# Kernel optimization log

Hardware: AMD Instinct MI355X
Metric: run time of the kernel (lower is better)

The kernel has to match this reference:

```python
import jax, jax.numpy as jnp
import numpy as np

B, T, M, D, O = 32, 4096, 256, 257, 40


def _make_cum_matrix():
    # 0/1 indicator: phone m covers a contiguous run of frames (segment-sum operator)
    seg_ids = (np.arange(T) * M) // T            # (T,) frame -> phone id
    ind = (seg_ids[None, :] == np.arange(M)[:, None]).astype(np.float32)  # (M,T)
    return jnp.broadcast_to(jnp.asarray(ind), (B, M, T))


def setup_inputs() -> dict:
    key = jax.random.key(0)
    k1, k2, k3, k4 = jax.random.split(key, 4)
    x = jax.random.normal(k1, (B, T, D), dtype=jnp.float32)
    # 0/1 phone-activity mask per frame/phone-class (as used via abs() in torch code)
    batch_target_phones = (jax.random.uniform(k2, (B, T, O)) < 0.5).astype(jnp.float32)
    batch_cum_matrix = _make_cum_matrix()
    W = jax.random.normal(k3, (O, D), dtype=jnp.float32) * 0.05
    b = jax.random.normal(k4, (O,), dtype=jnp.float32) * 0.05
    return {"x": x, "batch_target_phones": batch_target_phones,
            "batch_cum_matrix": batch_cum_matrix, "W": W, "b": b}


def reference(x, batch_target_phones, batch_cum_matrix, W, b):
    # summarize='mean' (generic non-'min' branch), loss_per_phone=True, eval=False
    # n_frames per phone, scattered back to frames as an extra feature column
    n_frames_by_phone = jnp.sum(batch_cum_matrix, axis=2)                     # (B, M)
    n_frames_2frame = jnp.einsum('bmt,bm->bt', batch_cum_matrix,
                                 n_frames_by_phone)[..., None]                # (B, T, 1)
    feats = jnp.concatenate([x[:, :, 1:], n_frames_2frame], axis=-1)          # (B, T, 257)
    out = jnp.einsum('btd,od->bto', feats, W) + b                             # (B, T, 40)
    masked = out * jnp.abs(batch_target_phones)                               # (B, T, 40)
    summed = jnp.einsum('bmt,bto->bmo', batch_cum_matrix, masked)             # (B, M, 40)
    frame_counts = jnp.einsum('bmt,bto->bmo', batch_cum_matrix,
                              batch_target_phones)                            # (B, M, 40)
    frame_counts = jnp.where(frame_counts == 0, 1.0, frame_counts)
    return summed / frame_counts                                              # (B, M, 40)
```

## Files before the change

### kernel.cpp

```cpp
#include <hip/hip_runtime.h>


#define B_  32
#define T_  4096
#define M_  256
#define D_  257
#define O_  40

#define NT    256
#define FPB   64
#define NSLOT 24

typedef float f32x4 __attribute__((ext_vector_type(4)));
typedef f32x4 f32x4u __attribute__((aligned(4)));
typedef _Float16 f16x8 __attribute__((ext_vector_type(8)));

__global__ __launch_bounds__(NT, 4) void ftdnn_mfma3(
    const float* __restrict__ x,
    const float* __restrict__ tp,
    const float* __restrict__ W,
    const float* __restrict__ bias,
    float* __restrict__ out)
{
    __shared__ __align__(16) _Float16 ws[NSLOT * 64 * 8];

    const int tid  = threadIdx.x;
    const int b    = blockIdx.y;
    const int mg   = blockIdx.x;
    const int lane = tid & 63;
    const int wv   = tid >> 6;
    const int ra   = lane & 15;
    const int kg   = lane >> 4;
    const int seg  = mg * 4 + wv;

    const float* xp = x + ((size_t)b * T_ + (size_t)seg * 16 + ra) * D_ + 1 + kg * 8;
    f32x4 xv[16];
#pragma unroll
    for (int kk = 0; kk < 8; ++kk) {
        const f32x4u* pv = reinterpret_cast<const f32x4u*>(xp + kk * 32);
        xv[2 * kk]     = pv[0];
        xv[2 * kk + 1] = pv[1];
    }
    const float* tpb = tp + ((size_t)b * T_ + (size_t)seg * 16) * O_;
    float tpv[3][4];
#pragma unroll
    for (int n = 0; n < 3; ++n) {
        const int o = n * 16 + ra;
#pragma unroll
        for (int r = 0; r < 4; ++r) {
            const int tl = kg * 4 + r;
            tpv[n][r] = (o < O_) ? tpb[(size_t)tl * O_ + o] : 0.f;
        }
    }
    float wcv[3], bsv[3];
#pragma unroll
    for (int n = 0; n < 3; ++n) {
        const int o = n * 16 + ra;
        wcv[n] = (o < O_) ? W[(size_t)o * D_ + 256] : 0.f;
        bsv[n] = (o < O_) ? bias[o] : 0.f;
    }

    for (int fid = tid; fid < NSLOT * 64; fid += NT) {
        const int slot = fid >> 6;
        const int ln   = fid & 63;
        const int n    = slot >> 3;
        const int kk   = slot & 7;
        const int o    = n * 16 + (ln & 15);
        const int k0   = kk * 32 + (ln >> 4) * 8;
        f16x8 h;
        if (o < O_) {
            const f32x4u* p = reinterpret_cast<const f32x4u*>(W + (size_t)o * D_ + k0);
            f32x4 d0 = p[0], d1 = p[1];
#pragma unroll
            for (int q = 0; q < 4; ++q) {
                h[q]     = (_Float16)d0[q];
                h[4 + q] = (_Float16)d1[q];
            }
        } else {
#pragma unroll
            for (int q = 0; q < 8; ++q) h[q] = (_Float16)0.f;
        }
        *reinterpret_cast<f16x8*>(&ws[fid * 8]) = h;
    }
    __syncthreads();

    const f16x8* wfrag = reinterpret_cast<const f16x8*>(ws);

    f32x4 acc[3];
#pragma unroll
    for (int n = 0; n < 3; ++n)
#pragma unroll
        for (int r = 0; r < 4; ++r) acc[n][r] = 0.f;

#pragma unroll
    for (int kk = 0; kk < 8; ++kk) {
        f32x4 d0 = xv[2 * kk];
        f32x4 d1 = xv[2 * kk + 1];
        f16x8 ah, al;
#pragma unroll
        for (int q = 0; q < 4; ++q) {
            ah[q]     = (_Float16)d0[q];
            al[q]     = (_Float16)(d0[q] - (float)ah[q]);
            ah[4 + q] = (_Float16)d1[q];
            al[4 + q] = (_Float16)(d1[q] - (float)ah[4 + q]);
        }
#pragma unroll
        for (int n = 0; n < 3; ++n) {
            f16x8 bh = wfrag[(n * 8 + kk) * 64 + lane];
            acc[n] = __builtin_amdgcn_mfma_f32_16x16x32_f16(ah, bh, acc[n], 0, 0, 0);
            acc[n] = __builtin_amdgcn_mfma_f32_16x16x32_f16(al, bh, acc[n], 0, 0, 0);
        }
    }

#pragma unroll
    for (int n = 0; n < 3; ++n) {
        const int o = n * 16 + ra;
        float s = 0.f, cnt = 0.f;
#pragma unroll
        for (int r = 0; r < 4; ++r) {
            s = fmaf(tpv[n][r], acc[n][r], s);
            cnt += tpv[n][r];
        }
        s   += __shfl_xor(s, 16);
        s   += __shfl_xor(s, 32);
        cnt += __shfl_xor(cnt, 16);
        cnt += __shfl_xor(cnt, 32);
        if (lane < 16 && o < O_) {
            float c     = fmaf(16.f, wcv[n], bsv[n]);
            float denom = (cnt == 0.f) ? 1.f : cnt;
            out[((size_t)b * M_ + seg) * O_ + o] = fmaf(c, cnt, s) / denom;
        }
    }
}

extern "C" void kernel_launch(void* const* d_in, const int* in_sizes, int n_in,
                              void* d_out, int out_size, void* d_ws, size_t ws_size,
                              hipStream_t stream) {
    const float* x    = (const float*)d_in[0];
    const float* tp   = (const float*)d_in[1];
    const float* W    = (const float*)d_in[3];
    const float* bias = (const float*)d_in[4];
    float* out        = (float*)d_out;

    dim3 grid(T_ / FPB, B_);
    dim3 block(NT);
    ftdnn_mfma3<<<grid, block, 0, stream>>>(x, tp, W, bias, out);
}
```

Measured before the change: 36.59 us.

## Process two segments per wave with software-pipelined x loads

Each wave now handles two 16-frame segments instead of one, which halves the grid and spreads the per-block W conversion into LDS over twice as much work. The x loads for the second segment are issued in halves while the MFMAs for the first segment run, overlapping global memory latency with compute. The cost is fewer blocks (1024 vs 2048), which lowers parallelism and occupancy headroom, plus slightly higher register pressure.

```diff
diff --git a/kernel.cpp b/kernel.cpp
--- a/kernel.cpp
+++ b/kernel.cpp
@@ -8,14 +8,13 @@
 #define O_  40
 
 #define NT    256
-#define FPB   64
 #define NSLOT 24
 
 typedef float f32x4 __attribute__((ext_vector_type(4)));
 typedef f32x4 f32x4u __attribute__((aligned(4)));
 typedef _Float16 f16x8 __attribute__((ext_vector_type(8)));
 
-__global__ __launch_bounds__(NT, 4) void ftdnn_mfma3(
+__global__ __launch_bounds__(NT, 4) void ftdnn_mfma4(
     const float* __restrict__ x,
     const float* __restrict__ tp,
     const float* __restrict__ W,
@@ -31,26 +30,29 @@
     const int wv   = tid >> 6;
     const int ra   = lane & 15;
     const int kg   = lane >> 4;
-    const int seg  = mg * 4 + wv;
+    const int s0   = mg * 8 + wv * 2;
 
-    const float* xp = x + ((size_t)b * T_ + (size_t)seg * 16 + ra) * D_ + 1 + kg * 8;
-    f32x4 xv[16];
+    const float* xp  = x + ((size_t)b * T_ + (size_t)s0 * 16 + ra) * D_ + 1 + kg * 8;
+    const float* tpb = tp + ((size_t)b * T_ + (size_t)s0 * 16) * O_;
+
+    f32x4 a0[8], a1[8];
 #pragma unroll
-    for (int kk = 0; kk < 8; ++kk) {
-        const f32x4u* pv = reinterpret_cast<const f32x4u*>(xp + kk * 32);
-        xv[2 * kk]     = pv[0];
-        xv[2 * kk + 1] = pv[1];
+    for (int i = 0; i < 4; ++i) {
+        const f32x4u* pv = reinterpret_cast<const f32x4u*>(xp + i * 32);
+        a0[2 * i] = pv[0];  a0[2 * i + 1] = pv[1];
     }
-    const float* tpb = tp + ((size_t)b * T_ + (size_t)seg * 16) * O_;
+#pragma unroll
+    for (int i = 0; i < 4; ++i) {
+        const f32x4u* pv = reinterpret_cast<const f32x4u*>(xp + 128 + i * 32);
+        a1[2 * i] = pv[0];  a1[2 * i + 1] = pv[1];
+    }
     float tpv[3][4];
 #pragma unroll
     for (int n = 0; n < 3; ++n) {
         const int o = n * 16 + ra;
 #pragma unroll
-        for (int r = 0; r < 4; ++r) {
-            const int tl = kg * 4 + r;
-            tpv[n][r] = (o < O_) ? tpb[(size_t)tl * O_ + o] : 0.f;
-        }
+        for (int r = 0; r < 4; ++r)
+            tpv[n][r] = (o < O_) ? tpb[(size_t)(kg * 4 + r) * O_ + o] : 0.f;
     }
     float wcv[3], bsv[3];
 #pragma unroll
@@ -86,51 +88,90 @@
 
     const f16x8* wfrag = reinterpret_cast<const f16x8*>(ws);
 
+    auto do_half = [&](const f32x4* av, int kkb, f32x4 (&acc)[3]) {
+#pragma unroll
+        for (int j = 0; j < 4; ++j) {
+            const int kk = kkb + j;
+            f32x4 d0 = av[2 * j];
+            f32x4 d1 = av[2 * j + 1];
+            f16x8 ah, al;
+#pragma unroll
+            for (int q = 0; q < 4; ++q) {
+                ah[q]     = (_Float16)d0[q];
+                al[q]     = (_Float16)(d0[q] - (float)ah[q]);
+                ah[4 + q] = (_Float16)d1[q];
+                al[4 + q] = (_Float16)(d1[q] - (float)ah[4 + q]);
+            }
+#pragma unroll
+            for (int n = 0; n < 3; ++n) {
+                f16x8 bh = wfrag[(n * 8 + kk) * 64 + lane];
+                acc[n] = __builtin_amdgcn_mfma_f32_16x16x32_f16(ah, bh, acc[n], 0, 0, 0);
+                acc[n] = __builtin_amdgcn_mfma_f32_16x16x32_f16(al, bh, acc[n], 0, 0, 0);
+            }
+        }
+    };
+
+    auto epilogue = [&](int seg, const f32x4 (&acc)[3], const float (&tpm)[3][4]) {
+#pragma unroll
+        for (int n = 0; n < 3; ++n) {
+            const int o = n * 16 + ra;
+            float s = 0.f, cnt = 0.f;
+#pragma unroll
+            for (int r = 0; r < 4; ++r) {
+                s = fmaf(tpm[n][r], acc[n][r], s);
+                cnt += tpm[n][r];
+            }
+            s   += __shfl_xor(s, 16);
+            s   += __shfl_xor(s, 32);
+            cnt += __shfl_xor(cnt, 16);
+            cnt += __shfl_xor(cnt, 32);
+            if (lane < 16 && o < O_) {
+                float c     = fmaf(16.f, wcv[n], bsv[n]);
+                float denom = (cnt == 0.f) ? 1.f : cnt;
+                out[((size_t)b * M_ + seg) * O_ + o] = fmaf(c, cnt, s) / denom;
+            }
+        }
+    };
+
     f32x4 acc[3];
 #pragma unroll
     for (int n = 0; n < 3; ++n)
 #pragma unroll
         for (int r = 0; r < 4; ++r) acc[n][r] = 0.f;
 
+    const float* xq = xp + (size_t)16 * D_;
+
+    do_half(a0, 0, acc);
 #pragma unroll
-    for (int kk = 0; kk < 8; ++kk) {
-        f32x4 d0 = xv[2 * kk];
-        f32x4 d1 = xv[2 * kk + 1];
-        f16x8 ah, al;
+    for (int i = 0; i < 4; ++i) {
+        const f32x4u* pv = reinterpret_cast<const f32x4u*>(xq + i * 32);
+        a0[2 * i] = pv[0];  a0[2 * i + 1] = pv[1];
+    }
+    do_half(a1, 4, acc);
 #pragma unroll
-        for (int q = 0; q < 4; ++q) {
-            ah[q]     = (_Float16)d0[q];
-            al[q]     = (_Float16)(d0[q] - (float)ah[q]);
-            ah[4 + q] = (_Float16)d1[q];
-            al[4 + q] = (_Float16)(d1[q] - (float)ah[4 + q]);
-        }
+    for (int i = 0; i < 4; ++i) {
+        const f32x4u* pv = reinterpret_cast<const f32x4u*>(xq + 128 + i * 32);
+        a1[2 * i] = pv[0];  a1[2 * i + 1] = pv[1];
+    }
+    epilogue(s0, acc, tpv);
+
+    const float* tpb1 = tpb + (size_t)16 * O_;
 #pragma unroll
-        for (int n = 0; n < 3; ++n) {
-            f16x8 bh = wfrag[(n * 8 + kk) * 64 + lane];
-            acc[n] = __builtin_amdgcn_mfma_f32_16x16x32_f16(ah, bh, acc[n], 0, 0, 0);
-            acc[n] = __builtin_amdgcn_mfma_f32_16x16x32_f16(al, bh, acc[n], 0, 0, 0);
-        }
+    for (int n = 0; n < 3; ++n) {
+        const int o = n * 16 + ra;
+#pragma unroll
+        for (int r = 0; r < 4; ++r)
+            tpv[n][r] = (o < O_) ? tpb1[(size_t)(kg * 4 + r) * O_ + o] : 0.f;
     }
 
 #pragma unroll
-    for (int n = 0; n < 3; ++n) {
-        const int o = n * 16 + ra;
-        float s = 0.f, cnt = 0.f;
+    for (int n = 0; n < 3; ++n)
 #pragma unroll
-        for (int r = 0; r < 4; ++r) {
-            s = fmaf(tpv[n][r], acc[n][r], s);
-            cnt += tpv[n][r];
-        }
-        s   += __shfl_xor(s, 16);
-        s   += __shfl_xor(s, 32);
-        cnt += __shfl_xor(cnt, 16);
-        cnt += __shfl_xor(cnt, 32);
-        if (lane < 16 && o < O_) {
-            float c     = fmaf(16.f, wcv[n], bsv[n]);
-            float denom = (cnt == 0.f) ? 1.f : cnt;
-            out[((size_t)b * M_ + seg) * O_ + o] = fmaf(c, cnt, s) / denom;
-        }
-    }
+        for (int r = 0; r < 4; ++r) acc[n][r] = 0.f;
+
+    do_half(a0, 0, acc);
+    do_half(a1, 4, acc);
+    epilogue(s0 + 1, acc, tpv);
 }
 
 extern "C" void kernel_launch(void* const* d_in, const int* in_sizes, int n_in,
@@ -142,7 +183,7 @@
     const float* bias = (const float*)d_in[4];
     float* out        = (float*)d_out;
 
-    dim3 grid(T_ / FPB, B_);
+    dim3 grid(32, 32);
     dim3 block(NT);
-    ftdnn_mfma3<<<grid, block, 0, stream>>>(x, tp, W, bias, out);
+    ftdnn_mfma4<<<grid, block, 0, stream>>>(x, tp, W, bias, out);
 }
```

After: 32.58 us. -11.0%, faster.

## Process two segments per wave with coalesced x loads staged through LDS and prefetch

Applied to the files above, without the earlier changes.

Each wave now handles two 16-frame segments instead of one, which halves the grid and amortizes the per-block W-to-fp16 staging. Rows of x are loaded with a more coalesced pattern (8 lanes per row, 4 floats each), split into hi/lo fp16 and written to per-wave LDS tiles, then read back in MFMA fragment layout. The next segment's x is prefetched while the current MFMAs run, and tp loads are moved late in the loop. The cost is extra LDS traffic, the wave-local LDS write/read ordering it depends on, and fewer blocks available to hide latency.

```diff
diff --git a/kernel.cpp b/kernel.cpp
--- a/kernel.cpp
+++ b/kernel.cpp
@@ -8,14 +8,16 @@
 #define O_  40
 
 #define NT    256
-#define FPB   64
+#define SEGW  2
 #define NSLOT 24
+#define XROWP 40
 
 typedef float f32x4 __attribute__((ext_vector_type(4)));
 typedef f32x4 f32x4u __attribute__((aligned(4)));
 typedef _Float16 f16x8 __attribute__((ext_vector_type(8)));
+typedef _Float16 f16x4 __attribute__((ext_vector_type(4)));
 
-__global__ __launch_bounds__(NT, 4) void ftdnn_mfma3(
+__global__ __launch_bounds__(NT, 4) void ftdnn_mfma6(
     const float* __restrict__ x,
     const float* __restrict__ tp,
     const float* __restrict__ W,
@@ -23,6 +25,8 @@
     float* __restrict__ out)
 {
     __shared__ __align__(16) _Float16 ws[NSLOT * 64 * 8];
+    __shared__ __align__(16) _Float16 xhi[4][16 * XROWP];
+    __shared__ __align__(16) _Float16 xlo[4][16 * XROWP];
 
     const int tid  = threadIdx.x;
     const int b    = blockIdx.y;
@@ -31,36 +35,11 @@
     const int wv   = tid >> 6;
     const int ra   = lane & 15;
     const int kg   = lane >> 4;
-    const int seg  = mg * 4 + wv;
+    const int s0   = mg * 8 + wv * 2;
 
-    const float* xp = x + ((size_t)b * T_ + (size_t)seg * 16 + ra) * D_ + 1 + kg * 8;
-    f32x4 xv[16];
 #pragma unroll
-    for (int kk = 0; kk < 8; ++kk) {
-        const f32x4u* pv = reinterpret_cast<const f32x4u*>(xp + kk * 32);
-        xv[2 * kk]     = pv[0];
-        xv[2 * kk + 1] = pv[1];
-    }
-    const float* tpb = tp + ((size_t)b * T_ + (size_t)seg * 16) * O_;
-    float tpv[3][4];
-#pragma unroll
-    for (int n = 0; n < 3; ++n) {
-        const int o = n * 16 + ra;
-#pragma unroll
-        for (int r = 0; r < 4; ++r) {
-            const int tl = kg * 4 + r;
-            tpv[n][r] = (o < O_) ? tpb[(size_t)tl * O_ + o] : 0.f;
-        }
-    }
-    float wcv[3], bsv[3];
-#pragma unroll
-    for (int n = 0; n < 3; ++n) {
-        const int o = n * 16 + ra;
-        wcv[n] = (o < O_) ? W[(size_t)o * D_ + 256] : 0.f;
-        bsv[n] = (o < O_) ? bias[o] : 0.f;
-    }
-
-    for (int fid = tid; fid < NSLOT * 64; fid += NT) {
+    for (int it = 0; it < 6; ++it) {
+        const int fid  = tid + it * NT;
         const int slot = fid >> 6;
         const int ln   = fid & 63;
         const int n    = slot >> 3;
@@ -84,51 +63,102 @@
     }
     __syncthreads();
 
-    const f16x8* wfrag = reinterpret_cast<const f16x8*>(ws);
+    const int wr = lane >> 3;
+    const int wc = lane & 7;
 
-    f32x4 acc[3];
-#pragma unroll
-    for (int n = 0; n < 3; ++n)
-#pragma unroll
-        for (int r = 0; r < 4; ++r) acc[n][r] = 0.f;
+    const float* xA = x + ((size_t)b * T_ + (size_t)s0 * 16 + wr) * D_ + 1 + wc * 4;
+    const float* xB = xA + (size_t)8 * D_;
 
+    f32x4 va[8], vb[8];
 #pragma unroll
     for (int kk = 0; kk < 8; ++kk) {
-        f32x4 d0 = xv[2 * kk];
-        f32x4 d1 = xv[2 * kk + 1];
-        f16x8 ah, al;
-#pragma unroll
-        for (int q = 0; q < 4; ++q) {
-            ah[q]     = (_Float16)d0[q];
-            al[q]     = (_Float16)(d0[q] - (float)ah[q]);
-            ah[4 + q] = (_Float16)d1[q];
-            al[4 + q] = (_Float16)(d1[q] - (float)ah[4 + q]);
-        }
-#pragma unroll
-        for (int n = 0; n < 3; ++n) {
-            f16x8 bh = wfrag[(n * 8 + kk) * 64 + lane];
-            acc[n] = __builtin_amdgcn_mfma_f32_16x16x32_f16(ah, bh, acc[n], 0, 0, 0);
-            acc[n] = __builtin_amdgcn_mfma_f32_16x16x32_f16(al, bh, acc[n], 0, 0, 0);
-        }
+        va[kk] = *reinterpret_cast<const f32x4u*>(xA + kk * 32);
+        vb[kk] = *reinterpret_cast<const f32x4u*>(xB + kk * 32);
     }
 
+    float wcv[3], bsv[3];
 #pragma unroll
     for (int n = 0; n < 3; ++n) {
         const int o = n * 16 + ra;
-        float s = 0.f, cnt = 0.f;
+        wcv[n] = (o < O_) ? W[(size_t)o * D_ + 256] : 0.f;
+        bsv[n] = (o < O_) ? bias[o] : 0.f;
+    }
+
+    const f16x8* wfrag = reinterpret_cast<const f16x8*>(ws);
+    _Float16* hib = xhi[wv];
+    _Float16* lob = xlo[wv];
+
 #pragma unroll
-        for (int r = 0; r < 4; ++r) {
-            s = fmaf(tpv[n][r], acc[n][r], s);
-            cnt += tpv[n][r];
+    for (int i = 0; i < SEGW; ++i) {
+        f32x4 acc[3];
+#pragma unroll
+        for (int n = 0; n < 3; ++n)
+#pragma unroll
+            for (int r = 0; r < 4; ++r) acc[n][r] = 0.f;
+
+        const float* xAn = xA + (size_t)(i + 1) * 16 * D_;
+        const float* xBn = xB + (size_t)(i + 1) * 16 * D_;
+        const float* tpb = tp + ((size_t)b * T_ + (size_t)(s0 + i) * 16) * O_;
+
+        float tpv[3][4];
+
+#pragma unroll
+        for (int kk = 0; kk < 8; ++kk) {
+            f32x4 da = va[kk];
+            f32x4 db = vb[kk];
+            f16x4 ha, la, hb, lb;
+#pragma unroll
+            for (int q = 0; q < 4; ++q) {
+                ha[q] = (_Float16)da[q];
+                la[q] = (_Float16)(da[q] - (float)ha[q]);
+                hb[q] = (_Float16)db[q];
+                lb[q] = (_Float16)(db[q] - (float)hb[q]);
+            }
+            *reinterpret_cast<f16x4*>(&hib[wr * XROWP + wc * 4])       = ha;
+            *reinterpret_cast<f16x4*>(&lob[wr * XROWP + wc * 4])       = la;
+            *reinterpret_cast<f16x4*>(&hib[(8 + wr) * XROWP + wc * 4]) = hb;
+            *reinterpret_cast<f16x4*>(&lob[(8 + wr) * XROWP + wc * 4]) = lb;
+            f16x8 ah = *reinterpret_cast<const f16x8*>(&hib[ra * XROWP + kg * 8]);
+            f16x8 al = *reinterpret_cast<const f16x8*>(&lob[ra * XROWP + kg * 8]);
+#pragma unroll
+            for (int n = 0; n < 3; ++n) {
+                f16x8 bh = wfrag[(n * 8 + kk) * 64 + lane];
+                acc[n] = __builtin_amdgcn_mfma_f32_16x16x32_f16(ah, bh, acc[n], 0, 0, 0);
+                acc[n] = __builtin_amdgcn_mfma_f32_16x16x32_f16(al, bh, acc[n], 0, 0, 0);
+            }
+            if (i + 1 < SEGW) {
+                va[kk] = *reinterpret_cast<const f32x4u*>(xAn + kk * 32);
+                vb[kk] = *reinterpret_cast<const f32x4u*>(xBn + kk * 32);
+            }
+            if (kk == 6) {
+#pragma unroll
+                for (int n = 0; n < 3; ++n) {
+                    const int o = n * 16 + ra;
+#pragma unroll
+                    for (int r = 0; r < 4; ++r)
+                        tpv[n][r] = (o < O_) ? tpb[(size_t)(kg * 4 + r) * O_ + o] : 0.f;
+                }
+            }
         }
-        s   += __shfl_xor(s, 16);
-        s   += __shfl_xor(s, 32);
-        cnt += __shfl_xor(cnt, 16);
-        cnt += __shfl_xor(cnt, 32);
-        if (lane < 16 && o < O_) {
-            float c     = fmaf(16.f, wcv[n], bsv[n]);
-            float denom = (cnt == 0.f) ? 1.f : cnt;
-            out[((size_t)b * M_ + seg) * O_ + o] = fmaf(c, cnt, s) / denom;
+
+#pragma unroll
+        for (int n = 0; n < 3; ++n) {
+            const int o = n * 16 + ra;
+            float s = 0.f, cnt = 0.f;
+#pragma unroll
+            for (int r = 0; r < 4; ++r) {
+                s = fmaf(tpv[n][r], acc[n][r], s);
+                cnt += tpv[n][r];
+            }
+            s   += __shfl_xor(s, 16);
+            s   += __shfl_xor(s, 32);
+            cnt += __shfl_xor(cnt, 16);
+            cnt += __shfl_xor(cnt, 32);
+            if (lane < 16 && o < O_) {
+                float c     = fmaf(16.f, wcv[n], bsv[n]);
+                float denom = (cnt == 0.f) ? 1.f : cnt;
+                out[((size_t)b * M_ + (s0 + i)) * O_ + o] = fmaf(c, cnt, s) / denom;
+            }
         }
     }
 }
@@ -142,7 +172,7 @@
     const float* bias = (const float*)d_in[4];
     float* out        = (float*)d_out;
 
-    dim3 grid(T_ / FPB, B_);
+    dim3 grid(32, 32);
     dim3 block(NT);
-    ftdnn_mfma3<<<grid, block, 0, stream>>>(x, tp, W, bias, out);
+    ftdnn_mfma6<<<grid, block, 0, stream>>>(x, tp, W, bias, out);
 }
```

Measured after the change: 34.65 us. 1.06x faster.

## Loop each wave over four segments with coalesced x loads staged through LDS

Applied to the files above, without the earlier changes.

Each wave now handles four 16-frame segments instead of one, which amortizes the per-block W fp16 conversion into LDS across four times as many segments and cuts the grid size by four. Rows of x are loaded with lane-contiguous, coalesced reads, converted to fp16 into a per-wave padded LDS tile, then read back in MFMA fragment layout. The next segment's x and tp values are prefetched into registers while the current one is computed. The hi/lo fp16 split of x is dropped, halving the MFMA count at the cost of accuracy, and launch bounds are relaxed to 2 blocks per CU, which may reduce occupancy.

```diff
diff --git a/kernel.cpp b/kernel.cpp
--- a/kernel.cpp
+++ b/kernel.cpp
@@ -8,14 +8,15 @@
 #define O_  40
 
 #define NT    256
-#define FPB   64
+#define SEGW  4
 #define NSLOT 24
+#define XP    264
 
 typedef float f32x4 __attribute__((ext_vector_type(4)));
 typedef f32x4 f32x4u __attribute__((aligned(4)));
 typedef _Float16 f16x8 __attribute__((ext_vector_type(8)));
 
-__global__ __launch_bounds__(NT, 4) void ftdnn_mfma3(
+__global__ __launch_bounds__(NT, 2) void ftdnn_mfma7(
     const float* __restrict__ x,
     const float* __restrict__ tp,
     const float* __restrict__ W,
@@ -23,6 +24,7 @@
     float* __restrict__ out)
 {
     __shared__ __align__(16) _Float16 ws[NSLOT * 64 * 8];
+    __shared__ __align__(16) _Float16 xs[4][16 * XP];
 
     const int tid  = threadIdx.x;
     const int b    = blockIdx.y;
@@ -31,26 +33,24 @@
     const int wv   = tid >> 6;
     const int ra   = lane & 15;
     const int kg   = lane >> 4;
-    const int seg  = mg * 4 + wv;
+    const int s0   = mg * 16 + wv * 4;
 
-    const float* xp = x + ((size_t)b * T_ + (size_t)seg * 16 + ra) * D_ + 1 + kg * 8;
-    f32x4 xv[16];
+    const float* xrow = x + ((size_t)b * T_ + (size_t)s0 * 16) * D_;
+    float xr[16][4];
 #pragma unroll
-    for (int kk = 0; kk < 8; ++kk) {
-        const f32x4u* pv = reinterpret_cast<const f32x4u*>(xp + kk * 32);
-        xv[2 * kk]     = pv[0];
-        xv[2 * kk + 1] = pv[1];
-    }
-    const float* tpb = tp + ((size_t)b * T_ + (size_t)seg * 16) * O_;
+    for (int r = 0; r < 16; ++r)
+#pragma unroll
+        for (int c = 0; c < 4; ++c)
+            xr[r][c] = xrow[(size_t)r * D_ + 1 + c * 64 + lane];
+
+    const float* tpb = tp + ((size_t)b * T_ + (size_t)s0 * 16) * O_;
     float tpv[3][4];
 #pragma unroll
     for (int n = 0; n < 3; ++n) {
         const int o = n * 16 + ra;
 #pragma unroll
-        for (int r = 0; r < 4; ++r) {
-            const int tl = kg * 4 + r;
-            tpv[n][r] = (o < O_) ? tpb[(size_t)tl * O_ + o] : 0.f;
-        }
+        for (int r = 0; r < 4; ++r)
+            tpv[n][r] = (o < O_) ? tpb[(size_t)(kg * 4 + r) * O_ + o] : 0.f;
     }
     float wcv[3], bsv[3];
 #pragma unroll
@@ -60,7 +60,9 @@
         bsv[n] = (o < O_) ? bias[o] : 0.f;
     }
 
-    for (int fid = tid; fid < NSLOT * 64; fid += NT) {
+#pragma unroll
+    for (int it = 0; it < 6; ++it) {
+        const int fid  = tid + it * NT;
         const int slot = fid >> 6;
         const int ln   = fid & 63;
         const int n    = slot >> 3;
@@ -85,50 +87,78 @@
     __syncthreads();
 
     const f16x8* wfrag = reinterpret_cast<const f16x8*>(ws);
-
-    f32x4 acc[3];
-#pragma unroll
-    for (int n = 0; n < 3; ++n)
-#pragma unroll
-        for (int r = 0; r < 4; ++r) acc[n][r] = 0.f;
+    _Float16* xb = xs[wv];
 
 #pragma unroll
-    for (int kk = 0; kk < 8; ++kk) {
-        f32x4 d0 = xv[2 * kk];
-        f32x4 d1 = xv[2 * kk + 1];
-        f16x8 ah, al;
+    for (int i = 0; i < SEGW; ++i) {
 #pragma unroll
-        for (int q = 0; q < 4; ++q) {
-            ah[q]     = (_Float16)d0[q];
-            al[q]     = (_Float16)(d0[q] - (float)ah[q]);
-            ah[4 + q] = (_Float16)d1[q];
-            al[4 + q] = (_Float16)(d1[q] - (float)ah[4 + q]);
+        for (int r = 0; r < 16; ++r)
+#pragma unroll
+            for (int c = 0; c < 4; ++c)
+                xb[r * XP + c * 64 + lane] = (_Float16)xr[r][c];
+
+        if (i + 1 < SEGW) {
+            const float* xn = xrow + (size_t)(i + 1) * 16 * D_;
+#pragma unroll
+            for (int r = 0; r < 16; ++r)
+#pragma unroll
+                for (int c = 0; c < 4; ++c)
+                    xr[r][c] = xn[(size_t)r * D_ + 1 + c * 64 + lane];
         }
+        float tpn[3][4];
+        if (i + 1 < SEGW) {
+            const float* tpn_p = tpb + (size_t)(i + 1) * 16 * O_;
+#pragma unroll
+            for (int n = 0; n < 3; ++n) {
+                const int o = n * 16 + ra;
+#pragma unroll
+                for (int r = 0; r < 4; ++r)
+                    tpn[n][r] = (o < O_) ? tpn_p[(size_t)(kg * 4 + r) * O_ + o] : 0.f;
+            }
+        }
+
+        f16x8 F[8];
+#pragma unroll
+        for (int kk = 0; kk < 8; ++kk)
+            F[kk] = *reinterpret_cast<const f16x8*>(&xb[ra * XP + kk * 32 + kg * 8]);
+
+        f32x4 acc[3];
+#pragma unroll
+        for (int n = 0; n < 3; ++n)
+#pragma unroll
+            for (int r = 0; r < 4; ++r) acc[n][r] = 0.f;
+#pragma unroll
+        for (int kk = 0; kk < 8; ++kk)
+#pragma unroll
+            for (int n = 0; n < 3; ++n)
+                acc[n] = __builtin_amdgcn_mfma_f32_16x16x32_f16(
+                             F[kk], wfrag[(n * 8 + kk) * 64 + lane], acc[n], 0, 0, 0);
+
 #pragma unroll
         for (int n = 0; n < 3; ++n) {
-            f16x8 bh = wfrag[(n * 8 + kk) * 64 + lane];
-            acc[n] = __builtin_amdgcn_mfma_f32_16x16x32_f16(ah, bh, acc[n], 0, 0, 0);
-            acc[n] = __builtin_amdgcn_mfma_f32_16x16x32_f16(al, bh, acc[n], 0, 0, 0);
+            const int o = n * 16 + ra;
+            float s = 0.f, cnt = 0.f;
+#pragma unroll
+            for (int r = 0; r < 4; ++r) {
+                s = fmaf(tpv[n][r], acc[n][r], s);
+                cnt += tpv[n][r];
+            }
+            s   += __shfl_xor(s, 16);
+            s   += __shfl_xor(s, 32);
+            cnt += __shfl_xor(cnt, 16);
+            cnt += __shfl_xor(cnt, 32);
+            if (lane < 16 && o < O_) {
+                float c     = fmaf(16.f, wcv[n], bsv[n]);
+                float denom = (cnt == 0.f) ? 1.f : cnt;
+                out[((size_t)b * M_ + (s0 + i)) * O_ + o] = fmaf(c, cnt, s) / denom;
+            }
         }
-    }
 
+        if (i + 1 < SEGW) {
 #pragma unroll
-    for (int n = 0; n < 3; ++n) {
-        const int o = n * 16 + ra;
-        float s = 0.f, cnt = 0.f;
+            for (int n = 0; n < 3; ++n)
 #pragma unroll
-        for (int r = 0; r < 4; ++r) {
-            s = fmaf(tpv[n][r], acc[n][r], s);
-            cnt += tpv[n][r];
-        }
-        s   += __shfl_xor(s, 16);
-        s   += __shfl_xor(s, 32);
-        cnt += __shfl_xor(cnt, 16);
-        cnt += __shfl_xor(cnt, 32);
-        if (lane < 16 && o < O_) {
-            float c     = fmaf(16.f, wcv[n], bsv[n]);
-            float denom = (cnt == 0.f) ? 1.f : cnt;
-            out[((size_t)b * M_ + seg) * O_ + o] = fmaf(c, cnt, s) / denom;
+                for (int r = 0; r < 4; ++r) tpv[n][r] = tpn[n][r];
         }
     }
 }
@@ -142,7 +172,7 @@
     const float* bias = (const float*)d_in[4];
     float* out        = (float*)d_out;
 
-    dim3 grid(T_ / FPB, B_);
+    dim3 grid(T_ / (16 * 4 * SEGW), B_);
     dim3 block(NT);
-    ftdnn_mfma3<<<grid, block, 0, stream>>>(x, tp, W, bias, out);
+    ftdnn_mfma7<<<grid, block, 0, stream>>>(x, tp, W, bias, out);
 }
```

New measurement: 34.38 us. 1.06x faster.
